# Optimization experiments

Hardware: AMD Instinct MI355X
Metric: run time of the kernel (lower is better)

Reference implementation:

```python
import jax, jax.numpy as jnp
import numpy as np

D_MODEL = 1024
N_HEAD = 16
D_HEAD = D_MODEL // N_HEAD
N_CTX = 2048
ROPE_BASE = 10000.0
SCALE = 1


def _rope_cache(seq_len, d_head, dtype=jnp.float32):
    inv_freq = 1.0 / (ROPE_BASE ** (jnp.arange(0, d_head, 2, dtype=jnp.float32) / d_head))
    t = jnp.arange(seq_len, dtype=jnp.float32)
    freqs = jnp.outer(t, inv_freq)              # [S, d_head/2]
    emb = jnp.concatenate([freqs, freqs], -1)   # [S, d_head]  (concat, per source)
    cos = jnp.cos(emb)[None, :, None, :].astype(dtype)
    sin = jnp.sin(emb)[None, :, None, :].astype(dtype)
    return cos, sin


def _apply_rope(x, cos, sin):
    # x: [B, S, H, Dh]; interleaved rotate (stack then flatten), per source
    x_even = x[..., 0::2]
    x_odd = x[..., 1::2]
    x_rot = jnp.stack([-x_odd, x_even], axis=-1).reshape(x.shape)
    return x * cos + x_rot * sin


def _rmsnorm(x, w):
    eps = jnp.finfo(x.dtype).eps  # torch RMSNorm default eps
    var = jnp.mean(jnp.square(x), axis=-1, keepdims=True)
    return x * jax.lax.rsqrt(var + eps) * w


def setup_inputs() -> dict:
    key = jax.random.key(0)
    ks = jax.random.split(key, 9)
    B, S = 2, N_CTX
    x = jax.random.normal(ks[0], (B, S, D_MODEL), jnp.float32)
    s = 0.02
    Wq = jax.random.normal(ks[1], (D_MODEL, D_MODEL), jnp.float32) * s
    bq = jax.random.normal(ks[2], (D_MODEL,), jnp.float32) * s
    Wk = jax.random.normal(ks[3], (D_MODEL, D_MODEL), jnp.float32) * s
    bk = jax.random.normal(ks[4], (D_MODEL,), jnp.float32) * s
    Wv = jax.random.normal(ks[5], (D_MODEL, D_MODEL), jnp.float32) * s
    bv = jax.random.normal(ks[6], (D_MODEL,), jnp.float32) * s
    Wo = jax.random.normal(ks[7], (D_MODEL, D_MODEL), jnp.float32) * s
    norm_w = jnp.ones((D_HEAD,), jnp.float32)
    return {"x": x, "Wq": Wq, "bq": bq, "Wk": Wk, "bk": bk,
            "Wv": Wv, "bv": bv, "Wo": Wo, "norm_w": norm_w}


def reference(x, Wq, bq, Wk, bk, Wv, bv, Wo, norm_w):
    B, S, _ = x.shape
    split = lambda t: t.reshape(B, S, N_HEAD, D_HEAD)
    q = split(x @ Wq.T + bq)
    k = split(x @ Wk.T + bk)
    v = split(x @ Wv.T + bv)
    cos, sin = _rope_cache(S, D_HEAD, x.dtype)
    q = _apply_rope(_rmsnorm(q, norm_w), cos, sin)
    k = _apply_rope(_rmsnorm(k, norm_w), cos, sin)
    scores = jnp.einsum('bqhd,bkhd->bhqk', q, k)
    causal = jnp.tril(jnp.ones((S, S), x.dtype))
    pattern = jnp.square(scores / D_HEAD) * causal  # quadratic score, masked
    z = jnp.einsum('bhqk,bkhd->bqhd', pattern, v).reshape(B, S, D_MODEL)
    return x + (z @ Wo.T) * SCALE
```

## Files before the change

kernel.cpp:

```cpp
#include <hip/hip_runtime.h>
#include <math.h>


typedef float  f32x4  __attribute__((ext_vector_type(4)));
typedef short  bf16x8 __attribute__((ext_vector_type(8)));
typedef float  vf4    __attribute__((ext_vector_type(4)));
typedef unsigned short u16x4 __attribute__((ext_vector_type(4)));

static __device__ __forceinline__ unsigned short f2bf(float f) {
    union { float f; unsigned int i; } c; c.f = f;
    unsigned int x = c.i;
    return (unsigned short)((x + 0x7fffu + ((x >> 16) & 1u)) >> 16);
}
static __device__ __forceinline__ f32x4 shfl_xor4(f32x4 v, int m) {
    f32x4 r;
    r[0] = __shfl_xor(v[0], m); r[1] = __shfl_xor(v[1], m);
    r[2] = __shfl_xor(v[2], m); r[3] = __shfl_xor(v[3], m);
    return r;
}
static __device__ __forceinline__ f32x4 rsq4(f32x4 v) {
    f32x4 r;
#pragma unroll
    for (int i = 0; i < 4; i++) r[i] = rsqrtf(v[i] * (1.0f / 64.0f) + 1.1920929e-07f);
    return r;
}
static __device__ __forceinline__ void cp16(const unsigned short* g, unsigned short* l) {
    __builtin_amdgcn_global_load_lds(
        (const __attribute__((address_space(1))) unsigned int*)g,
        (__attribute__((address_space(3))) unsigned int*)l, 16, 0, 0);
}

#define FOR_2(X)  X(0) X(1)
#define FOR_M(X)  X(0) X(1) X(2) X(3)
#define FOR_MN(X) X(0,0) X(0,1) X(0,2) X(0,3) X(1,0) X(1,1) X(1,2) X(1,3) \
                  X(2,0) X(2,1) X(2,2) X(2,3) X(3,0) X(3,1) X(3,2) X(3,3)
#define FOR_MN2(X) X(0,0) X(0,1) X(0,2) X(0,3) X(1,0) X(1,1) X(1,2) X(1,3)

#define MF(c,a,b) c = __builtin_amdgcn_mfma_f32_16x16x32_bf16(a, b, c, 0, 0, 0);

__global__ __launch_bounds__(256) void cvt_all(
    const float* __restrict__ x,  const float* __restrict__ Wq,
    const float* __restrict__ Wk, const float* __restrict__ Wv,
    const float* __restrict__ Wo,
    unsigned short* __restrict__ xb,  unsigned short* __restrict__ Wqb,
    unsigned short* __restrict__ Wkb, unsigned short* __restrict__ Wvb,
    unsigned short* __restrict__ Wob, int nx4, int nw4)
{
    int i = blockIdx.x * 256 + threadIdx.x;
    const float* s; unsigned short* d; int li;
    if (i < nx4) { s = x; d = xb; li = i; }
    else {
        int idx = i - nx4;
        int r = idx / nw4; li = idx - r * nw4;
        if (r >= 4) return;
        s = (r == 0) ? Wq : (r == 1) ? Wk : (r == 2) ? Wv : Wo;
        d = (r == 0) ? Wqb : (r == 1) ? Wkb : (r == 2) ? Wvb : Wob;
    }
    vf4 v = *(const vf4*)(s + (size_t)li * 4);
    u16x4 o;
#pragma unroll
    for (int j = 0; j < 4; j++) o[j] = f2bf(v[j]);
    *(u16x4*)(d + (size_t)li * 4) = o;
}

#define SS 136

__global__ __launch_bounds__(256, 3) void gemm_qkvz(
    const unsigned short* __restrict__ xb,
    const unsigned short* __restrict__ Wqb,
    const unsigned short* __restrict__ Wkb,
    const unsigned short* __restrict__ Wvb,
    const float* __restrict__ bqf, const float* __restrict__ bkf, const float* __restrict__ bvf,
    const float* __restrict__ nwp,
    unsigned short* __restrict__ qb, unsigned short* __restrict__ kb,
    unsigned short* __restrict__ vT)
{
    const int K = 1024;
    __shared__ unsigned short smem[17408];
    const int z = blockIdx.z;
    const unsigned short* Wb = (z == 0) ? Wqb : (z == 1) ? Wkb : Wvb;
    const float* bias = (z == 0) ? bqf : (z == 1) ? bkf : bvf;
    const int tid = threadIdx.x;
    const int n0 = blockIdx.x * 128;
    const int m0 = blockIdx.y * 128;
    const int lane = tid & 63, wid = tid >> 6;
    const int wy = wid >> 1, wx = wid & 1;
    const int l15 = lane & 15, quad = lane >> 4;
    const int r16 = lane >> 2;
    const int c8  = (lane & 3) * 8;

#define Z_DECL_ACC(mi,ni) f32x4 c##mi##ni = {0.f, 0.f, 0.f, 0.f};
    FOR_MN(Z_DECL_ACC)

#define Z_STAGE(BUF, KT) { \
        unsigned short* dstb = smem + (BUF) * 8192; \
        _Pragma("unroll") \
        for (int j = 0; j < 4; j++) { \
            const int ch = wid * 4 + j;           \
            const int mat = ch >> 3;              \
            const int row = (ch & 7) * 16 + r16; \
            const unsigned short* g = mat \
                ? Wb + (size_t)(n0 + row) * K + (KT) + c8 \
                : xb + (size_t)(m0 + row) * K + (KT) + c8; \
            cp16(g, &dstb[ch * 512]); \
        } }

#define Z_COMPUTE(BUF) { \
        const unsigned short* As_ = smem + (BUF) * 8192; \
        const unsigned short* Bs_ = As_ + 4096; \
        const bf16x8 a0 = *(const bf16x8*)&As_[(wy * 64 +  0 + l15) * 32 + quad * 8]; \
        const bf16x8 a1 = *(const bf16x8*)&As_[(wy * 64 + 16 + l15) * 32 + quad * 8]; \
        const bf16x8 a2 = *(const bf16x8*)&As_[(wy * 64 + 32 + l15) * 32 + quad * 8]; \
        const bf16x8 a3 = *(const bf16x8*)&As_[(wy * 64 + 48 + l15) * 32 + quad * 8]; \
        const bf16x8 b0 = *(const bf16x8*)&Bs_[(wx * 64 +  0 + l15) * 32 + quad * 8]; \
        const bf16x8 b1 = *(const bf16x8*)&Bs_[(wx * 64 + 16 + l15) * 32 + quad * 8]; \
        const bf16x8 b2 = *(const bf16x8*)&Bs_[(wx * 64 + 32 + l15) * 32 + quad * 8]; \
        const bf16x8 b3 = *(const bf16x8*)&Bs_[(wx * 64 + 48 + l15) * 32 + quad * 8]; \
        MF(c00,a0,b0) MF(c01,a0,b1) MF(c02,a0,b2) MF(c03,a0,b3) \
        MF(c10,a1,b0) MF(c11,a1,b1) MF(c12,a1,b2) MF(c13,a1,b3) \
        MF(c20,a2,b0) MF(c21,a2,b1) MF(c22,a2,b2) MF(c23,a2,b3) \
        MF(c30,a3,b0) MF(c31,a3,b1) MF(c32,a3,b2) MF(c33,a3,b3) }

    Z_STAGE(0, 0)
    __syncthreads();

    for (int kt = 0; kt < K; kt += 64) {
        Z_STAGE(1, kt + 32)
        Z_COMPUTE(0)
        __syncthreads();
        if (kt + 64 < K) Z_STAGE(0, kt + 64)
        Z_COMPUTE(1)
        __syncthreads();
    }

    const float bs0 = bias[n0 + wx * 64 + l15];
    const float bs1 = bias[n0 + wx * 64 + 16 + l15];
    const float bs2 = bias[n0 + wx * 64 + 32 + l15];
    const float bs3 = bias[n0 + wx * 64 + 48 + l15];
#define Z_BIAS(mi) c##mi##0 += bs0; c##mi##1 += bs1; c##mi##2 += bs2; c##mi##3 += bs3;
    FOR_M(Z_BIAS)

    if (z < 2) {
        const float nww0 = nwp[l15],      nww1 = nwp[16 + l15];
        const float nww2 = nwp[32 + l15], nww3 = nwp[48 + l15];
        const float lf0 = expf(-(float)l15 * 0.28782313662425572f);
        const float lf1 = expf(-(float)(l15 + 16) * 0.28782313662425572f);

#define Z_S2(mi) f32x4 s2_##mi = c##mi##0*c##mi##0 + c##mi##1*c##mi##1 + \
                                 c##mi##2*c##mi##2 + c##mi##3*c##mi##3; \
        s2_##mi = s2_##mi + shfl_xor4(s2_##mi, 1); \
        s2_##mi = s2_##mi + shfl_xor4(s2_##mi, 2); \
        s2_##mi = s2_##mi + shfl_xor4(s2_##mi, 4); \
        s2_##mi = s2_##mi + shfl_xor4(s2_##mi, 8); \
        s2_##mi = rsq4(s2_##mi);
        FOR_M(Z_S2)

#define Z_ROPE_ONE(mi,ni,NW,CS,SN) { \
            float vn = c##mi##ni[r] * s2v[r] * NW; \
            float pt = __shfl_xor(vn, 1); \
            float rot = (lane & 1) ? pt : -pt; \
            smem[mrow * SS + wx * 64 + (ni) * 16 + l15] = f2bf((vn * (CS) + rot * (SN)) * 0.125f); }
#define Z_ROPE_MI(mi) { f32x4 s2v = s2_##mi; \
            _Pragma("unroll") \
            for (int r = 0; r < 4; r++) { \
                const int mrow = wy * 64 + (mi) * 16 + quad * 4 + r; \
                const float t = (float)((m0 + mrow) & 2047); \
                const float a0 = t * lf0, a1 = t * lf1; \
                const float cs0 = cosf(a0), sn0 = sinf(a0); \
                const float cs1 = cosf(a1), sn1 = sinf(a1); \
                Z_ROPE_ONE(mi,0,nww0,cs0,sn0) Z_ROPE_ONE(mi,1,nww1,cs1,sn1) \
                Z_ROPE_ONE(mi,2,nww2,cs0,sn0) Z_ROPE_ONE(mi,3,nww3,cs1,sn1) } }
        FOR_M(Z_ROPE_MI)

        __syncthreads();
        unsigned short* dst = z ? kb : qb;
#pragma unroll
        for (int it = 0; it < 8; it++) {
            const int linear = tid + it * 256;
            const int row = linear >> 4, cb = linear & 15;
            *(bf16x8*)(dst + (size_t)(m0 + row) * 1024 + n0 + cb * 8) =
                *(const bf16x8*)&smem[row * SS + cb * 8];
        }
    } else {
#define Z_VST(mi,ni) { _Pragma("unroll") \
            for (int r = 0; r < 4; r++) { \
                const int mrow = wy * 64 + (mi) * 16 + quad * 4 + r; \
                smem[(wx * 64 + (ni) * 16 + l15) * SS + mrow] = f2bf(c##mi##ni[r]); } }
        FOR_MN(Z_VST)
        __syncthreads();
        const int b = m0 >> 11, tok0 = m0 & 2047;
#pragma unroll
        for (int it = 0; it < 8; it++) {
            const int linear = tid + it * 256;
            const int rowd = linear >> 4, cb = linear & 15;
            const int head_g = (n0 >> 6) + (rowd >> 6);
            const int d = rowd & 63;
            *(bf16x8*)(vT + (((size_t)b * 16 + head_g) * 64 + d) * 2048 + tok0 + cb * 8) =
                *(const bf16x8*)&smem[rowd * SS + cb * 8];
        }
    }
}

__global__ __launch_bounds__(512) void gemm_out(
    const unsigned short* __restrict__ zb,
    const unsigned short* __restrict__ Wob,
    const float* __restrict__ x, float* __restrict__ out, int M)
{
    const int K = 1024;
    __shared__ unsigned short smem[16384];
    const int tid = threadIdx.x;
    const int n0 = blockIdx.x * 128;
    const int m0 = blockIdx.y * 128;
    const int lane = tid & 63, wid = tid >> 6;
    const int wy = wid >> 1, wx = wid & 1;
    const int l15 = lane & 15, quad = lane >> 4;
    const int r16 = lane >> 2;
    const int c8  = (lane & 3) * 8;

#define G_DECL_ACC(mi,ni) f32x4 c##mi##ni = {0.f, 0.f, 0.f, 0.f};
    FOR_MN2(G_DECL_ACC)

#define O_STAGE(BUF, KT) { \
        unsigned short* dstb = smem + (BUF) * 8192; \
        _Pragma("unroll") \
        for (int j = 0; j < 2; j++) { \
            const int ch = wid * 2 + j;           \
            const int mat = ch >> 3;              \
            const int row = (ch & 7) * 16 + r16; \
            const unsigned short* g = (mat == 0) \
                ? zb  + (size_t)(m0 + row) * K + (KT) + c8 \
                : Wob + (size_t)(n0 + row) * K + (KT) + c8; \
            cp16(g, &dstb[ch * 512]); \
        } }

#define O_COMPUTE(BUF) { \
        const unsigned short* As_ = smem + (BUF) * 8192; \
        const unsigned short* Ws_ = As_ + 4096; \
        const bf16x8 a0 = *(const bf16x8*)&As_[(wy * 32 +  0 + l15) * 32 + quad * 8]; \
        const bf16x8 a1 = *(const bf16x8*)&As_[(wy * 32 + 16 + l15) * 32 + quad * 8]; \
        const bf16x8 b0 = *(const bf16x8*)&Ws_[(wx * 64 +  0 + l15) * 32 + quad * 8]; \
        const bf16x8 b1 = *(const bf16x8*)&Ws_[(wx * 64 + 16 + l15) * 32 + quad * 8]; \
        const bf16x8 b2 = *(const bf16x8*)&Ws_[(wx * 64 + 32 + l15) * 32 + quad * 8]; \
        const bf16x8 b3 = *(const bf16x8*)&Ws_[(wx * 64 + 48 + l15) * 32 + quad * 8]; \
        MF(c00,a0,b0) MF(c01,a0,b1) MF(c02,a0,b2) MF(c03,a0,b3) \
        MF(c10,a1,b0) MF(c11,a1,b1) MF(c12,a1,b2) MF(c13,a1,b3) }

    O_STAGE(0, 0)
    __syncthreads();

    for (int kt = 0; kt < K; kt += 64) {
        O_STAGE(1, kt + 32)
        O_COMPUTE(0)
        __syncthreads();
        if (kt + 64 < K) O_STAGE(0, kt + 64)
        O_COMPUTE(1)
        __syncthreads();
    }

#define G_OUTST(mi,ni) { _Pragma("unroll") \
        for (int r = 0; r < 4; r++) { \
            const int m = m0 + wy * 32 + (mi) * 16 + quad * 4 + r; \
            const int n = n0 + wx * 64 + (ni) * 16 + l15; \
            out[(size_t)m * 1024 + n] = c##mi##ni[r] + x[(size_t)m * 1024 + n]; } }
    FOR_MN2(G_OUTST)
}

__global__ __launch_bounds__(256) void attn_mfma(
    const unsigned short* __restrict__ qb, const unsigned short* __restrict__ kb,
    const unsigned short* __restrict__ vT, unsigned short* __restrict__ zb)
{
    __shared__ unsigned short Qs[128 * 72];
    __shared__ unsigned short Ks[64 * 72];
    __shared__ unsigned short Vs[64 * 72];
    __shared__ unsigned short Pm[128 * 72];
    const int tid = threadIdx.x;
    const int qt = 15 - blockIdx.x;
    const int bh = blockIdx.y;
    const int b = bh >> 4, h = bh & 15;
    const int lane = tid & 63, wq = tid >> 6;
    const int l15 = lane & 15, quad = lane >> 4;
    const size_t tokbase = (size_t)b * 2048;
    const int q0 = qt * 128;

#pragma unroll
    for (int j = 0; j < 4; j++) {
        const int u = tid + j * 256;
        const int row = u >> 3, seg = (u & 7) * 8;
        bf16x8 v = *(const bf16x8*)(qb + (tokbase + q0 + row) * 1024 + h * 64 + seg);
        *(bf16x8*)&Qs[row * 72 + seg] = v;
    }
    __syncthreads();
    const bf16x8 aq00 = *(const bf16x8*)&Qs[(wq * 32 + l15) * 72 + quad * 8];
    const bf16x8 aq01 = *(const bf16x8*)&Qs[(wq * 32 + l15) * 72 + 32 + quad * 8];
    const bf16x8 aq10 = *(const bf16x8*)&Qs[(wq * 32 + 16 + l15) * 72 + quad * 8];
    const bf16x8 aq11 = *(const bf16x8*)&Qs[(wq * 32 + 16 + l15) * 72 + 32 + quad * 8];

    const int kr = tid >> 3;
    const int sg = (tid & 7) * 8;

    bf16x8 pk0, pk1, pv0, pv1;
#define A_GLB(KT) { \
        pk0 = *(const bf16x8*)(kb + (tokbase + (KT) * 64 + kr) * 1024 + h * 64 + sg); \
        pk1 = *(const bf16x8*)(kb + (tokbase + (KT) * 64 + kr + 32) * 1024 + h * 64 + sg); \
        pv0 = *(const bf16x8*)(vT + ((size_t)bh * 64 + kr) * 2048 + (KT) * 64 + sg); \
        pv1 = *(const bf16x8*)(vT + ((size_t)bh * 64 + kr + 32) * 2048 + (KT) * 64 + sg); }

#define A_DECL_Z(mi,n) f32x4 z_##mi##n = {0.f, 0.f, 0.f, 0.f};
    FOR_MN2(A_DECL_Z)

    const int nkt = 2 * qt + 2;
    A_GLB(0)
    for (int kt = 0; kt < nkt; kt++) {
        __syncthreads();
        *(bf16x8*)&Ks[kr * 72 + sg] = pk0;
        *(bf16x8*)&Ks[(kr + 32) * 72 + sg] = pk1;
        *(bf16x8*)&Vs[kr * 72 + sg] = pv0;
        *(bf16x8*)&Vs[(kr + 32) * 72 + sg] = pv1;
        __syncthreads();
        if (kt + 1 < nkt) A_GLB(kt + 1)

#define A_DECL_S(mi,n) f32x4 s_##mi##n = {0.f, 0.f, 0.f, 0.f};
        FOR_MN2(A_DECL_S)
#define A_QKH(KS, AQ0, AQ1) { \
        bf16x8 b0 = *(const bf16x8*)&Ks[(l15) * 72 + (KS) * 32 + quad * 8]; \
        bf16x8 b1 = *(const bf16x8*)&Ks[(16 + l15) * 72 + (KS) * 32 + quad * 8]; \
        bf16x8 b2 = *(const bf16x8*)&Ks[(32 + l15) * 72 + (KS) * 32 + quad * 8]; \
        bf16x8 b3 = *(const bf16x8*)&Ks[(48 + l15) * 72 + (KS) * 32 + quad * 8]; \
        s_00 = __builtin_amdgcn_mfma_f32_16x16x32_bf16(AQ0, b0, s_00, 0, 0, 0); \
        s_01 = __builtin_amdgcn_mfma_f32_16x16x32_bf16(AQ0, b1, s_01, 0, 0, 0); \
        s_02 = __builtin_amdgcn_mfma_f32_16x16x32_bf16(AQ0, b2, s_02, 0, 0, 0); \
        s_03 = __builtin_amdgcn_mfma_f32_16x16x32_bf16(AQ0, b3, s_03, 0, 0, 0); \
        s_10 = __builtin_amdgcn_mfma_f32_16x16x32_bf16(AQ1, b0, s_10, 0, 0, 0); \
        s_11 = __builtin_amdgcn_mfma_f32_16x16x32_bf16(AQ1, b1, s_11, 0, 0, 0); \
        s_12 = __builtin_amdgcn_mfma_f32_16x16x32_bf16(AQ1, b2, s_12, 0, 0, 0); \
        s_13 = __builtin_amdgcn_mfma_f32_16x16x32_bf16(AQ1, b3, s_13, 0, 0, 0); }
        A_QKH(0, aq00, aq10)
        A_QKH(1, aq01, aq11)

        const bool needmask = (kt >= 2 * qt);
#define A_PSTORE(mi,n) { \
        f32x4 p4 = s_##mi##n * s_##mi##n; \
        if (needmask) { _Pragma("unroll") \
            for (int r = 0; r < 4; r++) \
                if (kt * 64 + (n) * 16 + l15 > q0 + wq * 32 + (mi) * 16 + quad * 4 + r) p4[r] = 0.f; } \
        _Pragma("unroll") \
        for (int r = 0; r < 4; r++) \
            Pm[(wq * 32 + (mi) * 16 + quad * 4 + r) * 72 + (n) * 16 + l15] = f2bf(p4[r]); }
        FOR_MN2(A_PSTORE)

#define A_PVH(KS) { \
        bf16x8 ap0 = *(const bf16x8*)&Pm[(wq * 32 + l15) * 72 + (KS) * 32 + quad * 8]; \
        bf16x8 ap1 = *(const bf16x8*)&Pm[(wq * 32 + 16 + l15) * 72 + (KS) * 32 + quad * 8]; \
        bf16x8 u0 = *(const bf16x8*)&Vs[(l15) * 72 + (KS) * 32 + quad * 8]; \
        bf16x8 u1 = *(const bf16x8*)&Vs[(16 + l15) * 72 + (KS) * 32 + quad * 8]; \
        bf16x8 u2 = *(const bf16x8*)&Vs[(32 + l15) * 72 + (KS) * 32 + quad * 8]; \
        bf16x8 u3 = *(const bf16x8*)&Vs[(48 + l15) * 72 + (KS) * 32 + quad * 8]; \
        z_00 = __builtin_amdgcn_mfma_f32_16x16x32_bf16(ap0, u0, z_00, 0, 0, 0); \
        z_01 = __builtin_amdgcn_mfma_f32_16x16x32_bf16(ap0, u1, z_01, 0, 0, 0); \
        z_02 = __builtin_amdgcn_mfma_f32_16x16x32_bf16(ap0, u2, z_02, 0, 0, 0); \
        z_03 = __builtin_amdgcn_mfma_f32_16x16x32_bf16(ap0, u3, z_03, 0, 0, 0); \
        z_10 = __builtin_amdgcn_mfma_f32_16x16x32_bf16(ap1, u0, z_10, 0, 0, 0); \
        z_11 = __builtin_amdgcn_mfma_f32_16x16x32_bf16(ap1, u1, z_11, 0, 0, 0); \
        z_12 = __builtin_amdgcn_mfma_f32_16x16x32_bf16(ap1, u2, z_12, 0, 0, 0); \
        z_13 = __builtin_amdgcn_mfma_f32_16x16x32_bf16(ap1, u3, z_13, 0, 0, 0); }
        A_PVH(0)
        A_PVH(1)
    }

#define A_ZST(mi,n) { _Pragma("unroll") \
        for (int r = 0; r < 4; r++) \
            Pm[(wq * 32 + (mi) * 16 + quad * 4 + r) * 72 + (n) * 16 + l15] = f2bf(z_##mi##n[r]); }
    FOR_MN2(A_ZST)
#pragma unroll
    for (int it = 0; it < 4; it++) {
        const int linear = it * 64 + lane;
        const int row = linear >> 3, cb = linear & 7;
        *(bf16x8*)(zb + (tokbase + q0 + wq * 32 + row) * 1024 + h * 64 + cb * 8) =
            *(const bf16x8*)&Pm[(wq * 32 + row) * 72 + cb * 8];
    }
}

extern "C" void kernel_launch(void* const* d_in, const int* in_sizes, int n_in,
                              void* d_out, int out_size, void* d_ws, size_t ws_size,
                              hipStream_t stream)
{
    const float* x  = (const float*)d_in[0];
    const float* Wq = (const float*)d_in[1];
    const float* bq = (const float*)d_in[2];
    const float* Wk = (const float*)d_in[3];
    const float* bk = (const float*)d_in[4];
    const float* Wv = (const float*)d_in[5];
    const float* bv = (const float*)d_in[6];
    const float* Wo = (const float*)d_in[7];
    const float* nw = (const float*)d_in[8];
    float* out = (float*)d_out;

    const int D = 1024;
    const int M = in_sizes[0] / D;

    unsigned short* xbb = (unsigned short*)d_ws;
    unsigned short* Wqb = xbb + (size_t)M * D;
    unsigned short* Wkb = Wqb + (size_t)D * D;
    unsigned short* Wvb = Wkb + (size_t)D * D;
    unsigned short* Wob = Wvb + (size_t)D * D;
    unsigned short* qbw = Wob + (size_t)D * D;
    unsigned short* kbw = qbw + (size_t)M * D;
    unsigned short* vTw = kbw + (size_t)M * D;
    unsigned short* zbw = vTw + (size_t)M * D;

    const int nx4 = M * D / 4, nw4 = D * D / 4;
    const int ncvt = nx4 + 4 * nw4;
    cvt_all<<<(ncvt + 255) / 256, 256, 0, stream>>>(
        x, Wq, Wk, Wv, Wo, xbb, Wqb, Wkb, Wvb, Wob, nx4, nw4);

    gemm_qkvz<<<dim3(D / 128, M / 128, 3), 256, 0, stream>>>(
        xbb, Wqb, Wkb, Wvb, bq, bk, bv, nw, qbw, kbw, vTw);

    attn_mfma<<<dim3(16, (M / 2048) * 16), 256, 0, stream>>>(qbw, kbw, vTw, zbw);

    gemm_out<<<dim3(D / 128, M / 128), 512, 0, stream>>>(zbw, Wob, x, out, M);
}
```

Measured before the change: 211.6 us.

## Triple-buffer GEMM K-loop with one barrier per step and explicit vmcnt waits

Both projection GEMMs (QKV and output) move from double-buffered shared memory with two __syncthreads per 64-wide K step to a three-stage ring. Each 32-wide step now uses a single s_barrier, and an explicit vmcnt wait lets one stage of async global loads stay in flight while the current stage is computed. This is meant to hide global-load latency and halve barrier count. In exchange it raises shared memory per block, which may lower occupancy in the launch_bounds(256,3) QKV kernel. It also depends on exact counts of outstanding loads for correctness.

```diff
diff --git a/kernel.cpp b/kernel.cpp
--- a/kernel.cpp
+++ b/kernel.cpp
@@ -76,7 +76,7 @@
     unsigned short* __restrict__ vT)
 {
     const int K = 1024;
-    __shared__ unsigned short smem[17408];
+    __shared__ unsigned short smem[24576];
     const int z = blockIdx.z;
     const unsigned short* Wb = (z == 0) ? Wqb : (z == 1) ? Wkb : Wvb;
     const float* bias = (z == 0) ? bqf : (z == 1) ? bkf : bvf;
@@ -122,16 +122,23 @@
         MF(c30,a3,b0) MF(c31,a3,b1) MF(c32,a3,b2) MF(c33,a3,b3) }
 
     Z_STAGE(0, 0)
+    Z_STAGE(1, 32)
+    {
+        int cbuf = 0, sbuf = 2;
+        for (int it = 0; it < 31; ++it) {
+            asm volatile("s_waitcnt vmcnt(4)" ::: "memory");
+            __builtin_amdgcn_s_barrier();
+            if (it < 30) { Z_STAGE(sbuf, (it + 2) * 32) }
+            Z_COMPUTE(cbuf)
+            asm volatile("s_waitcnt lgkmcnt(0)" ::: "memory");
+            cbuf = (cbuf == 2) ? 0 : cbuf + 1;
+            sbuf = (sbuf == 2) ? 0 : sbuf + 1;
+        }
+        asm volatile("s_waitcnt vmcnt(0)" ::: "memory");
+        __builtin_amdgcn_s_barrier();
+        Z_COMPUTE(cbuf)
+    }
     __syncthreads();
-
-    for (int kt = 0; kt < K; kt += 64) {
-        Z_STAGE(1, kt + 32)
-        Z_COMPUTE(0)
-        __syncthreads();
-        if (kt + 64 < K) Z_STAGE(0, kt + 64)
-        Z_COMPUTE(1)
-        __syncthreads();
-    }
 
     const float bs0 = bias[n0 + wx * 64 + l15];
     const float bs1 = bias[n0 + wx * 64 + 16 + l15];
@@ -207,7 +214,7 @@
     const float* __restrict__ x, float* __restrict__ out, int M)
 {
     const int K = 1024;
-    __shared__ unsigned short smem[16384];
+    __shared__ unsigned short smem[24576];
     const int tid = threadIdx.x;
     const int n0 = blockIdx.x * 128;
     const int m0 = blockIdx.y * 128;
@@ -246,15 +253,21 @@
         MF(c10,a1,b0) MF(c11,a1,b1) MF(c12,a1,b2) MF(c13,a1,b3) }
 
     O_STAGE(0, 0)
-    __syncthreads();
-
-    for (int kt = 0; kt < K; kt += 64) {
-        O_STAGE(1, kt + 32)
-        O_COMPUTE(0)
-        __syncthreads();
-        if (kt + 64 < K) O_STAGE(0, kt + 64)
-        O_COMPUTE(1)
-        __syncthreads();
+    O_STAGE(1, 32)
+    {
+        int cbuf = 0, sbuf = 2;
+        for (int it = 0; it < 31; ++it) {
+            asm volatile("s_waitcnt vmcnt(2)" ::: "memory");
+            __builtin_amdgcn_s_barrier();
+            if (it < 30) { O_STAGE(sbuf, (it + 2) * 32) }
+            O_COMPUTE(cbuf)
+            asm volatile("s_waitcnt lgkmcnt(0)" ::: "memory");
+            cbuf = (cbuf == 2) ? 0 : cbuf + 1;
+            sbuf = (sbuf == 2) ? 0 : sbuf + 1;
+        }
+        asm volatile("s_waitcnt vmcnt(0)" ::: "memory");
+        __builtin_amdgcn_s_barrier();
+        O_COMPUTE(cbuf)
     }
 
 #define G_OUTST(mi,ni) { _Pragma("unroll") \
```

Measured after the change: 211.1 us. No clear change (-0.2%).
